# Kernel optimization log

Measured on AMD Instinct MI355X. Metric: run time of the kernel, lower is better.

Reference implementation:

```python
import jax, jax.numpy as jnp
import numpy as np

S = 4096
E = 1024
H = 16
HD = E // H


def setup_inputs() -> dict:
    key = jax.random.key(0)
    k_x, k_wqkv, k_wo = jax.random.split(key, 3)
    x = jax.random.normal(k_x, (S, E), dtype=jnp.float32)
    # xavier_uniform for weights, zero biases (as in _reset_parameters)
    lim_qkv = np.sqrt(6.0 / (E + 3 * E)).astype(np.float32)
    Wqkv = jax.random.uniform(k_wqkv, (3 * E, E), minval=-lim_qkv, maxval=lim_qkv, dtype=jnp.float32)
    bqkv = jnp.zeros((3 * E,), dtype=jnp.float32)
    lim_o = np.sqrt(6.0 / (E + E)).astype(np.float32)
    Wo = jax.random.uniform(k_wo, (E, E), minval=-lim_o, maxval=lim_o, dtype=jnp.float32)
    bo = jnp.zeros((E,), dtype=jnp.float32)
    return {"x": x, "Wqkv": Wqkv, "bqkv": bqkv, "Wo": Wo, "bo": bo}


def reference(x, Wqkv, bqkv, Wo, bo):
    # QKV projection: [S, 3E]
    qkv = x @ Wqkv.T + bqkv
    # [S, H, 3*HD] -> [H, S, 3*HD]
    qkv = qkv.reshape(S, H, 3 * HD).transpose(1, 0, 2)
    q, k, v = jnp.split(qkv, 3, axis=-1)  # each [H, S, HD]
    scale = 1.0 / np.sqrt(HD).astype(np.float32)
    logits = jnp.einsum('hqd,hkd->hqk', q, k) * scale  # [H, S, S]
    attn = jax.nn.softmax(logits, axis=-1)
    values = jnp.einsum('hqk,hkd->hqd', attn, v)  # [H, S, HD]
    values = values.transpose(1, 0, 2).reshape(S, E)
    o = values @ Wo.T + bo
    return o
```

## Files before the change

kernel.cpp:

```cpp
#include <hip/hip_runtime.h>
#include <hip/hip_bf16.h>
#include <math.h>


#define S_LEN 4096
#define EMB   1024
#define NHEAD 16
#define HDIM  64
#define LDQ   3072

typedef __bf16 bf16x8 __attribute__((ext_vector_type(8)));
typedef unsigned short u16x8 __attribute__((ext_vector_type(8)));
typedef unsigned short u16x4 __attribute__((ext_vector_type(4)));
typedef short          s16x4 __attribute__((ext_vector_type(4)));
typedef float  f32x4  __attribute__((ext_vector_type(4)));

__device__ __forceinline__ unsigned short bf_bits(__hip_bfloat16 h) {
  return __builtin_bit_cast(unsigned short, h);
}
__device__ __forceinline__ bf16x8 ld_frag(const unsigned short* p) {
  return __builtin_bit_cast(bf16x8, *(const u16x8*)p);
}
__device__ __forceinline__ u16x4 pack4(float a, float b, float c, float d) {
  const __hip_bfloat162 p0 = __float22bfloat162_rn(make_float2(a, b));
  const __hip_bfloat162 p1 = __float22bfloat162_rn(make_float2(c, d));
  u16x4 r;
  r[0] = bf_bits(p0.x); r[1] = bf_bits(p0.y);
  r[2] = bf_bits(p1.x); r[3] = bf_bits(p1.y);
  return r;
}
__device__ __forceinline__ s16x4 cvt4(const f32x4 p) {
  unsigned int lo, hi;
  asm("v_cvt_pk_bf16_f32 %0, %1, %2" : "=v"(lo) : "v"(p[0]), "v"(p[1]));
  asm("v_cvt_pk_bf16_f32 %0, %1, %2" : "=v"(hi) : "v"(p[2]), "v"(p[3]));
  unsigned long long u = ((unsigned long long)hi << 32) | lo;
  return __builtin_bit_cast(s16x4, u);
}
__device__ __forceinline__ void gload_lds16(const unsigned short* g, unsigned short* l) {
  __builtin_amdgcn_global_load_lds(
      (const __attribute__((address_space(1))) unsigned int*)(const void*)g,
      (__attribute__((address_space(3))) unsigned int*)(void*)l, 16, 0, 0);
}

__global__ __launch_bounds__(256)
void cvt_bf16(const float* __restrict__ in, unsigned short* __restrict__ out) {
  const size_t i = ((size_t)blockIdx.x * 256 + threadIdx.x) * 8;
  const f32x4 lo = *(const f32x4*)(in + i);
  const f32x4 hi = *(const f32x4*)(in + i + 4);
  const u16x4 l4 = pack4(lo[0], lo[1], lo[2], lo[3]);
  const u16x4 h4 = pack4(hi[0], hi[1], hi[2], hi[3]);
  u16x8 r;
#pragma unroll
  for (int j = 0; j < 4; ++j) { r[j] = l4[j]; r[4 + j] = h4[j]; }
  *(u16x8*)(out + i) = r;
}

__global__ __launch_bounds__(256)
void gemm_qkv(const unsigned short* __restrict__ A,
              const unsigned short* __restrict__ B,
              const float* __restrict__ bias,
              unsigned short* __restrict__ qkv, unsigned short* __restrict__ Vt) {
  __shared__ __align__(16) unsigned short As[128 * 32];
  __shared__ __align__(16) unsigned short Bs[128 * 32];
  const int t      = threadIdx.x;
  const int w      = t >> 6;
  const int lane16 = t & 15;
  const int quad   = (t & 63) >> 4;
  const int wm = w >> 1, wn = w & 1;
  const int bm = blockIdx.y, bn = blockIdx.x;

  const size_t aoff = (size_t)(bm * 128 + (t >> 2)) * 1024 + (t & 3) * 8;
  const size_t boff = (size_t)(bn * 128 + (t >> 2)) * 1024 + (t & 3) * 8;
  unsigned short* asw = &As[w * 512];
  unsigned short* bsw = &Bs[w * 512];

  f32x4 acc[4][4] = {};

  for (int k0 = 0; k0 < 1024; k0 += 32) {
    __syncthreads();
    gload_lds16(A + aoff + k0,         asw);
    gload_lds16(A + aoff + k0 + 65536, asw + 2048);
    gload_lds16(B + boff + k0,         bsw);
    gload_lds16(B + boff + k0 + 65536, bsw + 2048);
    __syncthreads();

    bf16x8 af[4], bfr[4];
#pragma unroll
    for (int mt = 0; mt < 4; ++mt)
      af[mt] = ld_frag(&As[(wm * 64 + mt * 16 + lane16) * 32 + quad * 8]);
#pragma unroll
    for (int nt = 0; nt < 4; ++nt)
      bfr[nt] = ld_frag(&Bs[(wn * 64 + nt * 16 + lane16) * 32 + quad * 8]);
#pragma unroll
    for (int mt = 0; mt < 4; ++mt)
#pragma unroll
      for (int nt = 0; nt < 4; ++nt)
        acc[mt][nt] = __builtin_amdgcn_mfma_f32_16x16x32_bf16(af[mt], bfr[nt], acc[mt][nt], 0, 0, 0);
  }

  const int crow0 = bm * 128 + wm * 64;
  const int ccol0 = bn * 128 + wn * 64;
#pragma unroll
  for (int nt = 0; nt < 4; ++nt) {
    const int col = ccol0 + nt * 16 + lane16;
    const int segbase = (ccol0 + nt * 16) % 192;
    const float bv = bias[col];
    if (segbase < 128) {
      const float scale = (segbase < 64) ? 0.18033688011112042f : 1.0f;
#pragma unroll
      for (int mt = 0; mt < 4; ++mt)
#pragma unroll
        for (int r = 0; r < 4; ++r) {
          const int row = crow0 + mt * 16 + quad * 4 + r;
          qkv[(size_t)row * LDQ + col] = bf_bits(__float2bfloat16((acc[mt][nt][r] + bv) * scale));
        }
    } else {
      const int h = col / 192;
      const int d = (col % 192) - 128;
#pragma unroll
      for (int mt = 0; mt < 4; ++mt) {
        const int s0 = crow0 + mt * 16 + quad * 4;
        *(u16x4*)&Vt[(size_t)(h * 64 + d) * S_LEN + s0] =
            pack4(acc[mt][nt][0] + bv, acc[mt][nt][1] + bv,
                  acc[mt][nt][2] + bv, acc[mt][nt][3] + bv);
      }
    }
  }
}

__global__ __launch_bounds__(256)
void gemm_out(const unsigned short* __restrict__ A,
              const unsigned short* __restrict__ B,
              const float* __restrict__ bias,
              float* __restrict__ C) {
  __shared__ __align__(16) unsigned short As[128 * 32];
  __shared__ __align__(16) unsigned short Bs[128 * 32];
  const int t      = threadIdx.x;
  const int w      = t >> 6;
  const int lane16 = t & 15;
  const int quad   = (t & 63) >> 4;
  const int wm = w >> 1, wn = w & 1;
  const int bm = blockIdx.y, bn = blockIdx.x;

  const size_t aoff = (size_t)(bm * 128 + (t >> 2)) * 1024 + (t & 3) * 8;
  const size_t boff = (size_t)(bn * 128 + (t >> 2)) * 1024 + (t & 3) * 8;
  unsigned short* asw = &As[w * 512];
  unsigned short* bsw = &Bs[w * 512];

  f32x4 acc[4][4] = {};

  for (int k0 = 0; k0 < 1024; k0 += 32) {
    __syncthreads();
    gload_lds16(A + aoff + k0,         asw);
    gload_lds16(A + aoff + k0 + 65536, asw + 2048);
    gload_lds16(B + boff + k0,         bsw);
    gload_lds16(B + boff + k0 + 65536, bsw + 2048);
    __syncthreads();

    bf16x8 af[4], bfr[4];
#pragma unroll
    for (int mt = 0; mt < 4; ++mt)
      af[mt] = ld_frag(&As[(wm * 64 + mt * 16 + lane16) * 32 + quad * 8]);
#pragma unroll
    for (int nt = 0; nt < 4; ++nt)
      bfr[nt] = ld_frag(&Bs[(wn * 64 + nt * 16 + lane16) * 32 + quad * 8]);
#pragma unroll
    for (int mt = 0; mt < 4; ++mt)
#pragma unroll
      for (int nt = 0; nt < 4; ++nt)
        acc[mt][nt] = __builtin_amdgcn_mfma_f32_16x16x32_bf16(af[mt], bfr[nt], acc[mt][nt], 0, 0, 0);
  }

  const int crow0 = bm * 128 + wm * 64;
  const int ccol0 = bn * 128 + wn * 64;
#pragma unroll
  for (int nt = 0; nt < 4; ++nt) {
    const int col = ccol0 + nt * 16 + lane16;
    const float bv = bias[col];
#pragma unroll
    for (int mt = 0; mt < 4; ++mt)
#pragma unroll
      for (int r = 0; r < 4; ++r) {
        const int row = crow0 + mt * 16 + quad * 4 + r;
        C[(size_t)row * 1024 + col] = acc[mt][nt][r] + bv;
      }
  }
}

__global__ __launch_bounds__(256)
void attn_fwd(const unsigned short* __restrict__ qkv,
              const unsigned short* __restrict__ Vt,
              unsigned short* __restrict__ vals) {
  __shared__ __align__(16) unsigned short Ks[2][64 * 72];
  __shared__ __align__(16) unsigned short Vs[2][64 * 68];

  const int t      = threadIdx.x;
  const int w      = t >> 6;
  const int lane16 = t & 15;
  const int quad   = (t & 63) >> 4;
  const int h      = blockIdx.x & 15;
  const int qrow0  = (blockIdx.x >> 4) * 128 + w * 32;

  bf16x8 qf[2][2];
#pragma unroll
  for (int qb = 0; qb < 2; ++qb)
#pragma unroll
    for (int ks = 0; ks < 2; ++ks)
      qf[qb][ks] = ld_frag(&qkv[(size_t)(qrow0 + qb * 16 + lane16) * LDQ +
                                h * 192 + ks * 32 + quad * 8]);

  s16x4 ones;
#pragma unroll
  for (int i = 0; i < 4; ++i) ones[i] = (short)0x3F80;

  f32x4 ot[2][4] = {};
  f32x4 lacc[2]  = {};

  const int sn  = t >> 3;
  const int sd8 = (t & 7) * 8;
  const unsigned short* kbase = qkv + h * 192 + 64 + sd8;
  const unsigned short* vbase = Vt + (size_t)(h * 64 + sn) * S_LEN + sd8;

  u16x8 k0, k1, v0, v1;
  {
    const unsigned short* kp = kbase + (size_t)sn * LDQ;
    k0 = *(const u16x8*)kp;
    k1 = *(const u16x8*)(kp + (size_t)32 * LDQ);
    v0 = *(const u16x8*)vbase;
    v1 = *(const u16x8*)(vbase + (size_t)32 * S_LEN);
  }

  for (int kt = 0; kt < 64; ++kt) {
    const int b = kt & 1;
    unsigned short* ksb = &Ks[b][0];
    unsigned short* vsb = &Vs[b][0];
    *(u16x8*)&ksb[sn * 72 + sd8]        = k0;
    *(u16x8*)&ksb[(sn + 32) * 72 + sd8] = k1;
    {
      u16x4 a, bq, c, d;
#pragma unroll
      for (int j = 0; j < 4; ++j) { a[j] = v0[j]; bq[j] = v0[4 + j]; c[j] = v1[j]; d[j] = v1[4 + j]; }
      *(u16x4*)&vsb[sn * 68 + sd8]            = a;
      *(u16x4*)&vsb[sn * 68 + sd8 + 4]        = bq;
      *(u16x4*)&vsb[(sn + 32) * 68 + sd8]     = c;
      *(u16x4*)&vsb[(sn + 32) * 68 + sd8 + 4] = d;
    }
    if (kt != 63) {
      const unsigned short* kp = kbase + (size_t)((kt + 1) * 64 + sn) * LDQ;
      k0 = *(const u16x8*)kp;
      k1 = *(const u16x8*)(kp + (size_t)32 * LDQ);
      const unsigned short* vp = vbase + (kt + 1) * 64;
      v0 = *(const u16x8*)vp;
      v1 = *(const u16x8*)(vp + (size_t)32 * S_LEN);
    }
    __syncthreads();

    f32x4 s[2][4] = {};
#pragma unroll
    for (int nt = 0; nt < 4; ++nt)
#pragma unroll
      for (int ks = 0; ks < 2; ++ks) {
        const bf16x8 kf = ld_frag(&ksb[(nt * 16 + lane16) * 72 + ks * 32 + quad * 8]);
        s[0][nt] = __builtin_amdgcn_mfma_f32_16x16x32_bf16(kf, qf[0][ks], s[0][nt], 0, 0, 0);
        s[1][nt] = __builtin_amdgcn_mfma_f32_16x16x32_bf16(kf, qf[1][ks], s[1][nt], 0, 0, 0);
      }

    s16x4 pb[2][4];
#pragma unroll
    for (int qb = 0; qb < 2; ++qb)
#pragma unroll
      for (int c = 0; c < 4; ++c) {
        f32x4 p;
#pragma unroll
        for (int r = 0; r < 4; ++r) p[r] = exp2f(s[qb][c][r]);
        pb[qb][c] = cvt4(p);
        lacc[qb] = __builtin_amdgcn_mfma_f32_16x16x16bf16_1k(ones, pb[qb][c], lacc[qb], 0, 0, 0);
      }

#pragma unroll
    for (int c = 0; c < 4; ++c)
#pragma unroll
      for (int dt = 0; dt < 4; ++dt) {
        const s16x4 vf = __builtin_bit_cast(
            s16x4, *(const u16x4*)&vsb[(dt * 16 + lane16) * 68 + c * 16 + quad * 4]);
        ot[0][dt] = __builtin_amdgcn_mfma_f32_16x16x16bf16_1k(vf, pb[0][c], ot[0][dt], 0, 0, 0);
        ot[1][dt] = __builtin_amdgcn_mfma_f32_16x16x16bf16_1k(vf, pb[1][c], ot[1][dt], 0, 0, 0);
      }
  }

#pragma unroll
  for (int qb = 0; qb < 2; ++qb) {
    const float inv = 1.0f / lacc[qb][0];
    const int row = qrow0 + qb * 16 + lane16;
#pragma unroll
    for (int dt = 0; dt < 4; ++dt)
      *(u16x4*)&vals[(size_t)row * EMB + h * 64 + dt * 16 + quad * 4] =
          pack4(ot[qb][dt][0] * inv, ot[qb][dt][1] * inv,
                ot[qb][dt][2] * inv, ot[qb][dt][3] * inv);
  }
}

extern "C" void kernel_launch(void* const* d_in, const int* in_sizes, int n_in,
                              void* d_out, int out_size, void* d_ws, size_t ws_size,
                              hipStream_t stream) {
  (void)in_sizes; (void)n_in; (void)out_size; (void)ws_size;
  const float* x    = (const float*)d_in[0];
  const float* Wqkv = (const float*)d_in[1];
  const float* bqkv = (const float*)d_in[2];
  const float* Wo   = (const float*)d_in[3];
  const float* bo   = (const float*)d_in[4];

  unsigned short* qkv  = (unsigned short*)d_ws;
  unsigned short* vals = qkv + (size_t)S_LEN * LDQ;
  unsigned short* Vt   = vals + (size_t)S_LEN * EMB;
  unsigned short* xb   = Vt + (size_t)EMB * S_LEN;
  unsigned short* Wqb  = xb + (size_t)S_LEN * EMB;
  unsigned short* Wob  = Wqb + (size_t)3072 * 1024;

  dim3 blk(256);
  cvt_bf16<<<dim3(4096 * 1024 / 2048), blk, 0, stream>>>(x, xb);
  cvt_bf16<<<dim3(3072 * 1024 / 2048), blk, 0, stream>>>(Wqkv, Wqb);
  cvt_bf16<<<dim3(1024 * 1024 / 2048), blk, 0, stream>>>(Wo, Wob);

  gemm_qkv<<<dim3(3072 / 128, 4096 / 128), blk, 0, stream>>>(xb, Wqb, bqkv, qkv, Vt);
  attn_fwd<<<dim3((S_LEN / 128) * NHEAD), blk, 0, stream>>>(qkv, Vt, vals);
  gemm_out<<<dim3(1024 / 128, 4096 / 128), blk, 0, stream>>>(vals, Wob, bo, (float*)d_out);
}
```

Measured before the change: 259.8 us.

## Split attention block into 8 waves with 16 query rows each

The attention kernel now runs 512 threads per block, with each wave owning 16 query rows instead of 32. Each thread loads one K and one V row per tile instead of two. The aim is more waves in flight to hide latency and fewer registers per wave, with launch bounds requesting 4 blocks per CU. It also raises wave priority around the MFMA sections and switches to the hardware exp2 intrinsic. In exchange, each K/V fragment read from shared memory now feeds only one MFMA instead of two, so LDS traffic per FLOP doubles.

```diff
diff --git a/kernel.cpp b/kernel.cpp
--- a/kernel.cpp
+++ b/kernel.cpp
@@ -187,7 +187,7 @@
   }
 }
 
-__global__ __launch_bounds__(256)
+__global__ __launch_bounds__(512, 4)
 void attn_fwd(const unsigned short* __restrict__ qkv,
               const unsigned short* __restrict__ Vt,
               unsigned short* __restrict__ vals) {
@@ -199,105 +199,85 @@
   const int lane16 = t & 15;
   const int quad   = (t & 63) >> 4;
   const int h      = blockIdx.x & 15;
-  const int qrow0  = (blockIdx.x >> 4) * 128 + w * 32;
-
-  bf16x8 qf[2][2];
-#pragma unroll
-  for (int qb = 0; qb < 2; ++qb)
-#pragma unroll
-    for (int ks = 0; ks < 2; ++ks)
-      qf[qb][ks] = ld_frag(&qkv[(size_t)(qrow0 + qb * 16 + lane16) * LDQ +
-                                h * 192 + ks * 32 + quad * 8]);
+  const int qrow0  = (blockIdx.x >> 4) * 128 + w * 16;
+
+  bf16x8 qf[2];
+#pragma unroll
+  for (int ks = 0; ks < 2; ++ks)
+    qf[ks] = ld_frag(&qkv[(size_t)(qrow0 + lane16) * LDQ + h * 192 + ks * 32 + quad * 8]);
 
   s16x4 ones;
 #pragma unroll
   for (int i = 0; i < 4; ++i) ones[i] = (short)0x3F80;
 
-  f32x4 ot[2][4] = {};
-  f32x4 lacc[2]  = {};
+  f32x4 ot[4] = {};
+  f32x4 lacc  = {};
 
   const int sn  = t >> 3;
   const int sd8 = (t & 7) * 8;
   const unsigned short* kbase = qkv + h * 192 + 64 + sd8;
   const unsigned short* vbase = Vt + (size_t)(h * 64 + sn) * S_LEN + sd8;
 
-  u16x8 k0, k1, v0, v1;
-  {
-    const unsigned short* kp = kbase + (size_t)sn * LDQ;
-    k0 = *(const u16x8*)kp;
-    k1 = *(const u16x8*)(kp + (size_t)32 * LDQ);
-    v0 = *(const u16x8*)vbase;
-    v1 = *(const u16x8*)(vbase + (size_t)32 * S_LEN);
-  }
+  u16x8 k0 = *(const u16x8*)(kbase + (size_t)sn * LDQ);
+  u16x8 v0 = *(const u16x8*)vbase;
 
   for (int kt = 0; kt < 64; ++kt) {
     const int b = kt & 1;
     unsigned short* ksb = &Ks[b][0];
     unsigned short* vsb = &Vs[b][0];
-    *(u16x8*)&ksb[sn * 72 + sd8]        = k0;
-    *(u16x8*)&ksb[(sn + 32) * 72 + sd8] = k1;
+    *(u16x8*)&ksb[sn * 72 + sd8] = k0;
     {
-      u16x4 a, bq, c, d;
-#pragma unroll
-      for (int j = 0; j < 4; ++j) { a[j] = v0[j]; bq[j] = v0[4 + j]; c[j] = v1[j]; d[j] = v1[4 + j]; }
-      *(u16x4*)&vsb[sn * 68 + sd8]            = a;
-      *(u16x4*)&vsb[sn * 68 + sd8 + 4]        = bq;
-      *(u16x4*)&vsb[(sn + 32) * 68 + sd8]     = c;
-      *(u16x4*)&vsb[(sn + 32) * 68 + sd8 + 4] = d;
+      u16x4 a, bq;
+#pragma unroll
+      for (int j = 0; j < 4; ++j) { a[j] = v0[j]; bq[j] = v0[4 + j]; }
+      *(u16x4*)&vsb[sn * 68 + sd8]     = a;
+      *(u16x4*)&vsb[sn * 68 + sd8 + 4] = bq;
     }
     if (kt != 63) {
-      const unsigned short* kp = kbase + (size_t)((kt + 1) * 64 + sn) * LDQ;
-      k0 = *(const u16x8*)kp;
-      k1 = *(const u16x8*)(kp + (size_t)32 * LDQ);
-      const unsigned short* vp = vbase + (kt + 1) * 64;
-      v0 = *(const u16x8*)vp;
-      v1 = *(const u16x8*)(vp + (size_t)32 * S_LEN);
+      k0 = *(const u16x8*)(kbase + (size_t)((kt + 1) * 64 + sn) * LDQ);
+      v0 = *(const u16x8*)(vbase + (kt + 1) * 64);
     }
     __syncthreads();
 
-    f32x4 s[2][4] = {};
+    f32x4 s[4] = {};
+    __builtin_amdgcn_s_setprio(1);
 #pragma unroll
     for (int nt = 0; nt < 4; ++nt)
 #pragma unroll
       for (int ks = 0; ks < 2; ++ks) {
         const bf16x8 kf = ld_frag(&ksb[(nt * 16 + lane16) * 72 + ks * 32 + quad * 8]);
-        s[0][nt] = __builtin_amdgcn_mfma_f32_16x16x32_bf16(kf, qf[0][ks], s[0][nt], 0, 0, 0);
-        s[1][nt] = __builtin_amdgcn_mfma_f32_16x16x32_bf16(kf, qf[1][ks], s[1][nt], 0, 0, 0);
+        s[nt] = __builtin_amdgcn_mfma_f32_16x16x32_bf16(kf, qf[ks], s[nt], 0, 0, 0);
       }
-
-    s16x4 pb[2][4];
-#pragma unroll
-    for (int qb = 0; qb < 2; ++qb)
-#pragma unroll
-      for (int c = 0; c < 4; ++c) {
-        f32x4 p;
-#pragma unroll
-        for (int r = 0; r < 4; ++r) p[r] = exp2f(s[qb][c][r]);
-        pb[qb][c] = cvt4(p);
-        lacc[qb] = __builtin_amdgcn_mfma_f32_16x16x16bf16_1k(ones, pb[qb][c], lacc[qb], 0, 0, 0);
-      }
-
+    __builtin_amdgcn_s_setprio(0);
+
+    s16x4 pb[4];
+#pragma unroll
+    for (int c = 0; c < 4; ++c) {
+      f32x4 p;
+#pragma unroll
+      for (int r = 0; r < 4; ++r) p[r] = __builtin_amdgcn_exp2f(s[c][r]);
+      pb[c] = cvt4(p);
+      lacc = __builtin_amdgcn_mfma_f32_16x16x16bf16_1k(ones, pb[c], lacc, 0, 0, 0);
+    }
+
+    __builtin_amdgcn_s_setprio(1);
 #pragma unroll
     for (int c = 0; c < 4; ++c)
 #pragma unroll
       for (int dt = 0; dt < 4; ++dt) {
         const s16x4 vf = __builtin_bit_cast(
             s16x4, *(const u16x4*)&vsb[(dt * 16 + lane16) * 68 + c * 16 + quad * 4]);
-        ot[0][dt] = __builtin_amdgcn_mfma_f32_16x16x16bf16_1k(vf, pb[0][c], ot[0][dt], 0, 0, 0);
-        ot[1][dt] = __builtin_amdgcn_mfma_f32_16x16x16bf16_1k(vf, pb[1][c], ot[1][dt], 0, 0, 0);
+        ot[dt] = __builtin_amdgcn_mfma_f32_16x16x16bf16_1k(vf, pb[c], ot[dt], 0, 0, 0);
       }
-  }
-
-#pragma unroll
-  for (int qb = 0; qb < 2; ++qb) {
-    const float inv = 1.0f / lacc[qb][0];
-    const int row = qrow0 + qb * 16 + lane16;
-#pragma unroll
-    for (int dt = 0; dt < 4; ++dt)
-      *(u16x4*)&vals[(size_t)row * EMB + h * 64 + dt * 16 + quad * 4] =
-          pack4(ot[qb][dt][0] * inv, ot[qb][dt][1] * inv,
-                ot[qb][dt][2] * inv, ot[qb][dt][3] * inv);
-  }
+    __builtin_amdgcn_s_setprio(0);
+  }
+
+  const float inv = 1.0f / lacc[0];
+  const int row = qrow0 + lane16;
+#pragma unroll
+  for (int dt = 0; dt < 4; ++dt)
+    *(u16x4*)&vals[(size_t)row * EMB + h * 64 + dt * 16 + quad * 4] =
+        pack4(ot[dt][0] * inv, ot[dt][1] * inv, ot[dt][2] * inv, ot[dt][3] * inv);
 }
 
 extern "C" void kernel_launch(void* const* d_in, const int* in_sizes, int n_in,
@@ -323,6 +303,6 @@
   cvt_bf16<<<dim3(1024 * 1024 / 2048), blk, 0, stream>>>(Wo, Wob);
 
   gemm_qkv<<<dim3(3072 / 128, 4096 / 128), blk, 0, stream>>>(xb, Wqb, bqkv, qkv, Vt);
-  attn_fwd<<<dim3((S_LEN / 128) * NHEAD), blk, 0, stream>>>(qkv, Vt, vals);
+  attn_fwd<<<dim3((S_LEN / 128) * NHEAD), dim3(512), 0, stream>>>(qkv, Vt, vals);
   gemm_out<<<dim3(1024 / 128, 4096 / 128), blk, 0, stream>>>(vals, Wob, bo, (float*)d_out);
 }
```

New measurement: 230.5 us. -11.3%, faster.
